# Performance work log

Measured on AMD Instinct MI355X. Metric: run time of the kernel, lower is better.

The kernel has to match this reference:

```python
import jax, jax.numpy as jnp
import numpy as np

B, T, C, H = 2, 2048, 1024, 16
HD = C // H
MAX_WAVELENGTH = 10000.0


def apply_rope(x, positions):
    # x: [B, H, T, HD], positions: [T]
    fraction = 2.0 * jnp.arange(HD // 2, dtype=jnp.float32) / HD
    timescale = MAX_WAVELENGTH ** fraction  # [HD//2]
    sinusoid = positions[:, None] / timescale[None, :]  # [T, HD//2]
    sin = jnp.sin(sinusoid)
    cos = jnp.cos(sinusoid)
    first, second = jnp.split(x, 2, axis=-1)
    out = jnp.concatenate(
        [first * cos - second * sin, second * cos + first * sin], axis=-1
    )
    return out.astype(x.dtype)


def setup_inputs() -> dict:
    key = jax.random.key(0)
    k1, k2, k3 = jax.random.split(key, 3)
    x = jax.random.normal(k1, (B, T, C), dtype=jnp.float32)
    w_attn = jax.random.normal(k2, (C, 3 * C), dtype=jnp.float32) * 0.02
    b_attn = jnp.zeros((3 * C,), dtype=jnp.float32)
    w_proj = jax.random.normal(k3, (C, C), dtype=jnp.float32) * 0.02
    b_proj = jnp.zeros((C,), dtype=jnp.float32)
    return {"x": x, "w_attn": w_attn, "b_attn": b_attn,
            "w_proj": w_proj, "b_proj": b_proj}


def reference(x, w_attn, b_attn, w_proj, b_proj):
    b, t, c = x.shape
    qkv = x @ w_attn + b_attn  # [B, T, 3C]
    q, k, v = jnp.split(qkv, 3, axis=-1)
    q = q.reshape(b, t, H, HD).transpose(0, 2, 1, 3)  # [B, H, T, HD]
    k = k.reshape(b, t, H, HD).transpose(0, 2, 1, 3)
    v = v.reshape(b, t, H, HD).transpose(0, 2, 1, 3)
    positions = jnp.arange(t, dtype=x.dtype)
    q = apply_rope(q, positions)
    k = apply_rope(k, positions)
    att = jnp.einsum('bhqd,bhkd->bhqk', q, k) * (1.0 / jnp.sqrt(HD))
    causal = jnp.tril(jnp.ones((t, t), dtype=bool))
    att = jnp.where(causal, att, jnp.finfo(att.dtype).min)
    att = jax.nn.softmax(att, axis=-1)
    y = jnp.einsum('bhqk,bhkd->bhqd', att, v)
    y = y.transpose(0, 2, 1, 3).reshape(b, t, c)
    return y @ w_proj + b_proj
```

## Files before the change

kernel.cpp:

```cpp
#include <hip/hip_runtime.h>
#include <hip/hip_bf16.h>


typedef __attribute__((ext_vector_type(8))) short short8;
typedef __attribute__((ext_vector_type(4))) float floatx4;

__device__ __forceinline__ unsigned short f2bf(float f) {
    union { float f; unsigned int u; } v; v.f = f;
    unsigned int r = v.u + 0x7FFFu + ((v.u >> 16) & 1u);
    return (unsigned short)(r >> 16);
}

__device__ __forceinline__ float bf2f(unsigned short u) {
    union { unsigned int u; float f; } v; v.u = ((unsigned int)u) << 16;
    return v.f;
}

__device__ __forceinline__ unsigned int pk2bf(float a, float b) {
    union { float f; unsigned int u; } ua, ub;
    ua.f = a; ub.f = b;
    return __builtin_amdgcn_perm(ub.u + 0x8000u, ua.u + 0x8000u, 0x07060302u);
}

__device__ __forceinline__ void gld16(const void* g, void* l) {
    __builtin_amdgcn_global_load_lds(
        (const __attribute__((address_space(1))) unsigned int*)g,
        (__attribute__((address_space(3))) unsigned int*)l, 16, 0, 0);
}

__global__ void cast_f32_bf16(const float* __restrict__ in,
                              unsigned short* __restrict__ out, int n4) {
    int i = blockIdx.x * blockDim.x + threadIdx.x;
    if (i < n4) {
        float4 v = ((const float4*)in)[i];
        ushort4 o;
        o.x = f2bf(v.x); o.y = f2bf(v.y); o.z = f2bf(v.z); o.w = f2bf(v.w);
        ((ushort4*)out)[i] = o;
    }
}

__global__ void transpose_cast(const float* __restrict__ in,
                               unsigned short* __restrict__ out,
                               int R, int NC) {
    __shared__ unsigned short tile[64][65];
    int r0 = blockIdx.y * 64;
    int c0 = blockIdx.x * 64;
    int t = threadIdx.x;
    int col = t & 63;
    int rr = t >> 6;
#pragma unroll
    for (int i = 0; i < 16; i++) {
        int row = rr + i * 4;
        tile[row][col] = f2bf(in[(size_t)(r0 + row) * NC + c0 + col]);
    }
    __syncthreads();
#pragma unroll
    for (int i = 0; i < 16; i++) {
        int orow = rr + i * 4;
        out[(size_t)(c0 + orow) * R + r0 + col] = tile[col][orow];
    }
}

template <int OUT_BF16>
__global__ __launch_bounds__(256) void gemm_lds(
    const unsigned short* __restrict__ A,
    const unsigned short* __restrict__ BT,
    const float* __restrict__ bias,
    void* __restrict__ out,
    int M, int N, int K) {
    __shared__ __align__(16) unsigned short as[128 * 64];
    __shared__ __align__(16) unsigned short bs[128 * 64];
    int lane = threadIdx.x & 63;
    int w = threadIdx.x >> 6;
    int wx = w & 1, wy = w >> 1;
    int l16 = lane & 15, quad = lane >> 4;
    int m0 = blockIdx.y * 128;
    int n0 = blockIdx.x * 128;
    int x = l16 & 7;
    int lr = lane >> 3;
    int gc = (lane & 7) ^ lr;

    floatx4 acc[4][4];
#pragma unroll
    for (int mi = 0; mi < 4; mi++)
#pragma unroll
        for (int ni = 0; ni < 4; ni++)
            acc[mi][ni] = (floatx4){0.f, 0.f, 0.f, 0.f};

    for (int k0 = 0; k0 < K; k0 += 64) {
        __syncthreads();
#pragma unroll
        for (int i = 0; i < 4; i++) {
            int seg = w * 4 + i;
            int row = seg * 8 + lr;
            gld16(A + (size_t)(m0 + row) * K + k0 + gc * 8, &as[seg * 512]);
            gld16(BT + (size_t)(n0 + row) * K + k0 + gc * 8, &bs[seg * 512]);
        }
        __syncthreads();
#pragma unroll
        for (int kk = 0; kk < 2; kk++) {
            short8 af[4], bf[4];
#pragma unroll
            for (int mi = 0; mi < 4; mi++) {
                int r = wy * 64 + mi * 16 + l16;
                af[mi] = *(const short8*)&as[r * 64 + (((kk << 2) | quad) ^ x) * 8];
            }
#pragma unroll
            for (int ni = 0; ni < 4; ni++) {
                int r = wx * 64 + ni * 16 + l16;
                bf[ni] = *(const short8*)&bs[r * 64 + (((kk << 2) | quad) ^ x) * 8];
            }
#pragma unroll
            for (int mi = 0; mi < 4; mi++)
#pragma unroll
                for (int ni = 0; ni < 4; ni++)
                    acc[mi][ni] = __builtin_amdgcn_mfma_f32_16x16x32_bf16(
                        af[mi], bf[ni], acc[mi][ni], 0, 0, 0);
        }
    }

#pragma unroll
    for (int mi = 0; mi < 4; mi++)
#pragma unroll
        for (int ni = 0; ni < 4; ni++) {
            int row = m0 + wy * 64 + mi * 16 + quad * 4;
            int col = n0 + wx * 64 + ni * 16 + l16;
            float bv = bias[col];
#pragma unroll
            for (int r = 0; r < 4; r++) {
                float v = acc[mi][ni][r] + bv;
                if (OUT_BF16)
                    ((unsigned short*)out)[(size_t)(row + r) * N + col] = f2bf(v);
                else
                    ((float*)out)[(size_t)(row + r) * N + col] = v;
            }
        }
}

__global__ void rope_reorg(const unsigned short* __restrict__ qkv,
                           unsigned short* __restrict__ qT,
                           unsigned short* __restrict__ kT) {
    int idx = blockIdx.x * 256 + threadIdx.x;
    int d = idx & 31;
    int h = (idx >> 5) & 15;
    int bt = idx >> 9;
    int t = bt & 2047;
    int b = bt >> 11;
    const unsigned short* row = qkv + (size_t)bt * 3072;
    float q1 = bf2f(row[h * 64 + d]);
    float q2 = bf2f(row[h * 64 + d + 32]);
    float k1 = bf2f(row[1024 + h * 64 + d]);
    float k2 = bf2f(row[1024 + h * 64 + d + 32]);
    float inv_ts = exp2f(-0.41524101186092036f * (float)d);
    float ang = (float)t * inv_ts;
    float s = sinf(ang), c = cosf(ang);
    size_t obase = ((size_t)(b * 16 + h) * 2048 + t) * 64 + d;
    qT[obase]      = f2bf((q1 * c - q2 * s) * 0.125f);
    qT[obase + 32] = f2bf((q2 * c + q1 * s) * 0.125f);
    kT[obase]      = f2bf(k1 * c - k2 * s);
    kT[obase + 32] = f2bf(k2 * c + k1 * s);
}

__global__ void v_transpose(const unsigned short* __restrict__ qkv,
                            unsigned short* __restrict__ vT) {
    __shared__ unsigned short tile[64][65];
    int bh = blockIdx.y;
    int b = bh >> 4, h = bh & 15;
    int t0 = blockIdx.x * 64;
    int tid = threadIdx.x;
    int col = tid & 63;
    int rr = tid >> 6;
#pragma unroll
    for (int i = 0; i < 16; i++) {
        int trow = rr + i * 4;
        tile[trow][col] =
            qkv[(size_t)(b * 2048 + t0 + trow) * 3072 + 2048 + h * 64 + col];
    }
    __syncthreads();
#pragma unroll
    for (int i = 0; i < 16; i++) {
        int drow = rr + i * 4;
        vT[((size_t)bh * 64 + drow) * 2048 + t0 + col] = tile[col][drow];
    }
}

__global__ __launch_bounds__(512) void attn4(
    const unsigned short* __restrict__ qT,
    const unsigned short* __restrict__ kT,
    const unsigned short* __restrict__ vT,
    unsigned short* __restrict__ y) {
    __shared__ __align__(16) unsigned short kbuf[2][64 * 64];
    __shared__ __align__(16) unsigned short vbuf[2][64 * 64];
    __shared__ __align__(16) unsigned short pl[8][16 * 88];
    int lane = threadIdx.x & 63;
    int w = threadIdx.x >> 6;
    int l16 = lane & 15, quad = lane >> 4;
    int blk = blockIdx.x;
    int idx = blk >> 5;
    int qb = (idx < 8) ? (15 - idx * 2) : ((idx - 8) * 2);
    int bh = blk & 31;
    int b = bh >> 4, h = bh & 15;
    int q0 = qb * 128 + w * 16;
    int dt = 2 * qb + (w >> 2);
    const unsigned short* qp = qT + (size_t)bh * 2048 * 64;
    const unsigned short* kp = kT + (size_t)bh * 2048 * 64;
    const unsigned short* vp = vT + (size_t)bh * 64 * 2048;
    unsigned short* plw = pl[w];
    int x = l16 & 7;

    short8 qf0 = *(const short8*)(qp + (size_t)(q0 + l16) * 64 + quad * 8);
    short8 qf1 = *(const short8*)(qp + (size_t)(q0 + l16) * 64 + 32 + quad * 8);

    floatx4 acc[4];
#pragma unroll
    for (int ni = 0; ni < 4; ni++) acc[ni] = (floatx4){0.f, 0.f, 0.f, 0.f};
    float l_part = 0.f;

    auto stage = [&](int bi, int j0) {
#pragma unroll
        for (int i = 0; i < 2; i++) {
            int t = w * 2 + i;
            if (t < 8) {
                int r = t * 8 + (lane >> 3);
                int c = (lane & 7) ^ (r & 7);
                gld16(kp + (size_t)(j0 + r) * 64 + c * 8, &kbuf[bi][t * 512]);
            } else {
                int s = t - 8;
                int d = s * 8 + (lane >> 3);
                int c = (lane & 7) ^ (d & 7);
                gld16(vp + (size_t)d * 2048 + j0 + c * 8, &vbuf[bi][s * 512]);
            }
        }
    };

    int L = 2 * qb + 2;
    stage(0, 0);
    for (int it = 0; it < L; it++) {
        int j0 = it * 64;
        int bi = it & 1;
        __syncthreads();
        if (it + 1 < L) stage(bi ^ 1, j0 + 64);
        if (it > dt) continue;
        const unsigned short* kb = kbuf[bi];
        const unsigned short* vb = vbuf[bi];
        bool diag = (it == dt);
        floatx4 s[4];
#pragma unroll
        for (int c = 0; c < 4; c++) {
            int r = c * 16 + l16;
            short8 kf0 = *(const short8*)&kb[r * 64 + ((quad) ^ x) * 8];
            short8 kf1 = *(const short8*)&kb[r * 64 + ((quad | 4) ^ x) * 8];
            floatx4 z = (floatx4){0.f, 0.f, 0.f, 0.f};
            z = __builtin_amdgcn_mfma_f32_16x16x32_bf16(kf0, qf0, z, 0, 0, 0);
            z = __builtin_amdgcn_mfma_f32_16x16x32_bf16(kf1, qf1, z, 0, 0, 0);
            s[c] = z;
        }
        int query = q0 + l16;
#pragma unroll
        for (int c = 0; c < 4; c++) {
            float p[4];
#pragma unroll
            for (int r = 0; r < 4; r++) {
                float e = __expf(s[c][r]);
                if (diag) {
                    int key = j0 + c * 16 + quad * 4 + r;
                    e = (key <= query) ? e : 0.f;
                }
                p[r] = e;
            }
            l_part += (p[0] + p[1]) + (p[2] + p[3]);
            uint2 pk = {pk2bf(p[0], p[1]), pk2bf(p[2], p[3])};
            *(uint2*)&plw[l16 * 88 + c * 16 + quad * 4] = pk;
        }
        short8 pa0 = *(const short8*)&plw[l16 * 88 + quad * 8];
        short8 pa1 = *(const short8*)&plw[l16 * 88 + 32 + quad * 8];
#pragma unroll
        for (int ni = 0; ni < 4; ni++) {
            int d = ni * 16 + l16;
            short8 vf0 = *(const short8*)&vb[d * 64 + ((quad) ^ x) * 8];
            short8 vf1 = *(const short8*)&vb[d * 64 + ((quad | 4) ^ x) * 8];
            acc[ni] = __builtin_amdgcn_mfma_f32_16x16x32_bf16(pa0, vf0, acc[ni], 0, 0, 0);
            acc[ni] = __builtin_amdgcn_mfma_f32_16x16x32_bf16(pa1, vf1, acc[ni], 0, 0, 0);
        }
    }

    float tot = l_part;
    tot += __shfl_xor(tot, 16, 64);
    tot += __shfl_xor(tot, 32, 64);
    float inv[4];
#pragma unroll
    for (int r = 0; r < 4; r++)
        inv[r] = 1.f / __shfl(tot, quad * 4 + r, 16);
#pragma unroll
    for (int ni = 0; ni < 4; ni++)
#pragma unroll
        for (int r = 0; r < 4; r++) {
            int t = q0 + quad * 4 + r;
            y[((size_t)(b * 2048 + t)) * 1024 + h * 64 + ni * 16 + l16] =
                f2bf(acc[ni][r] * inv[r]);
        }
}

extern "C" void kernel_launch(void* const* d_in, const int* in_sizes, int n_in,
                              void* d_out, int out_size, void* d_ws, size_t ws_size,
                              hipStream_t stream) {
    const float* x      = (const float*)d_in[0];
    const float* w_attn = (const float*)d_in[1];
    const float* b_attn = (const float*)d_in[2];
    const float* w_proj = (const float*)d_in[3];
    const float* b_proj = (const float*)d_in[4];
    float* out = (float*)d_out;

    char* ws = (char*)d_ws;
    unsigned short* x_bf = (unsigned short*)ws;
    unsigned short* wTa  = (unsigned short*)(ws + (8ull << 20));
    unsigned short* wTp  = (unsigned short*)(ws + (14ull << 20));
    unsigned short* qkv  = (unsigned short*)(ws + (16ull << 20));
    unsigned short* qTb  = (unsigned short*)(ws + (40ull << 20));
    unsigned short* kTb  = (unsigned short*)(ws + (48ull << 20));
    unsigned short* vTb  = (unsigned short*)(ws + (56ull << 20));
    unsigned short* y_bf = x_bf;

    cast_f32_bf16<<<4096, 256, 0, stream>>>(x, x_bf, 1048576);
    transpose_cast<<<dim3(48, 16), 256, 0, stream>>>(w_attn, wTa, 1024, 3072);
    transpose_cast<<<dim3(16, 16), 256, 0, stream>>>(w_proj, wTp, 1024, 1024);
    gemm_lds<1><<<dim3(24, 32), 256, 0, stream>>>(x_bf, wTa, b_attn, qkv,
                                                  4096, 3072, 1024);
    rope_reorg<<<8192, 256, 0, stream>>>(qkv, qTb, kTb);
    v_transpose<<<dim3(32, 32), 256, 0, stream>>>(qkv, vTb);
    attn4<<<512, 512, 0, stream>>>(qTb, kTb, vTb, y_bf);
    gemm_lds<0><<<dim3(8, 32), 256, 0, stream>>>(y_bf, wTp, b_proj, out,
                                                 4096, 1024, 1024);
}
```

Measured before the change: 201.0 us.

## Fuse RoPE and V transpose into QKV GEMM epilogue; narrow proj tiles

The QKV GEMM epilogue now applies the bias, RoPE (using a precomputed sin/cos table) and the q scaling, and writes Q and K straight into per-head layout. V is transposed through LDS and written as vT. This removes the intermediate qkv buffer and the separate rope_reorg and v_transpose kernels. The output projection GEMM switches to 128x64 tiles so that 512 blocks launch instead of 256, which improves CU occupancy. A small rope_tab kernel is added, and the fused epilogue uses scattered 2-byte stores for Q and K.

Measured after the change: 190.1 us. 1.06x faster.

```diff
diff --git a/kernel.cpp b/kernel.cpp
--- a/kernel.cpp
+++ b/kernel.cpp
@@ -11,11 +11,6 @@
     return (unsigned short)(r >> 16);
 }
 
-__device__ __forceinline__ float bf2f(unsigned short u) {
-    union { unsigned int u; float f; } v; v.u = ((unsigned int)u) << 16;
-    return v.f;
-}
-
 __device__ __forceinline__ unsigned int pk2bf(float a, float b) {
     union { float f; unsigned int u; } ua, ub;
     ua.f = a; ub.f = b;
@@ -26,6 +21,14 @@
     __builtin_amdgcn_global_load_lds(
         (const __attribute__((address_space(1))) unsigned int*)g,
         (__attribute__((address_space(3))) unsigned int*)l, 16, 0, 0);
+}
+
+__global__ void rope_tab(float2* __restrict__ tab) {
+    int i = blockIdx.x * 256 + threadIdx.x;
+    int t = i >> 5, d = i & 31;
+    float inv_ts = exp2f(-0.41524101186092036f * (float)d);
+    float ang = (float)t * inv_ts;
+    tab[i] = make_float2(sinf(ang), cosf(ang));
 }
 
 __global__ void cast_f32_bf16(const float* __restrict__ in,
@@ -61,17 +64,20 @@
     }
 }
 
-template <int OUT_BF16>
-__global__ __launch_bounds__(256) void gemm_lds(
+__global__ __launch_bounds__(256) void gemm_qkv(
     const unsigned short* __restrict__ A,
     const unsigned short* __restrict__ BT,
     const float* __restrict__ bias,
-    void* __restrict__ out,
-    int M, int N, int K) {
-    __shared__ __align__(16) unsigned short as[128 * 64];
-    __shared__ __align__(16) unsigned short bs[128 * 64];
-    int lane = threadIdx.x & 63;
-    int w = threadIdx.x >> 6;
+    const float2* __restrict__ tab,
+    unsigned short* __restrict__ qT,
+    unsigned short* __restrict__ kT,
+    unsigned short* __restrict__ vT) {
+    __shared__ __align__(16) unsigned short smem[16384];
+    unsigned short* as = smem;
+    unsigned short* bs = smem + 8192;
+    int tid = threadIdx.x;
+    int lane = tid & 63;
+    int w = tid >> 6;
     int wx = w & 1, wy = w >> 1;
     int l16 = lane & 15, quad = lane >> 4;
     int m0 = blockIdx.y * 128;
@@ -87,14 +93,14 @@
         for (int ni = 0; ni < 4; ni++)
             acc[mi][ni] = (floatx4){0.f, 0.f, 0.f, 0.f};
 
-    for (int k0 = 0; k0 < K; k0 += 64) {
+    for (int k0 = 0; k0 < 1024; k0 += 64) {
         __syncthreads();
 #pragma unroll
         for (int i = 0; i < 4; i++) {
             int seg = w * 4 + i;
             int row = seg * 8 + lr;
-            gld16(A + (size_t)(m0 + row) * K + k0 + gc * 8, &as[seg * 512]);
-            gld16(BT + (size_t)(n0 + row) * K + k0 + gc * 8, &bs[seg * 512]);
+            gld16(A + (size_t)(m0 + row) * 1024 + k0 + gc * 8, &as[seg * 512]);
+            gld16(BT + (size_t)(n0 + row) * 1024 + k0 + gc * 8, &bs[seg * 512]);
         }
         __syncthreads();
 #pragma unroll
@@ -119,69 +125,135 @@
         }
     }
 
+    int region = n0 >> 10;
+    int b = m0 >> 11;
+    float b0 = bias[n0 + wx * 64 + l16];
+    float b1 = bias[n0 + wx * 64 + 16 + l16];
+    float b2 = bias[n0 + wx * 64 + 32 + l16];
+    float b3 = bias[n0 + wx * 64 + 48 + l16];
+
+    if (region < 2) {
+        unsigned short* qk = region ? kT : qT;
+        float scale = region ? 1.0f : 0.125f;
+        int h = ((n0 & 1023) + wx * 64) >> 6;
+        unsigned short* obase = qk + (size_t)(b * 16 + h) * 2048 * 64;
+#pragma unroll
+        for (int mi = 0; mi < 4; mi++)
+#pragma unroll
+            for (int r = 0; r < 4; r++) {
+                int t = (m0 & 2047) + wy * 64 + mi * 16 + quad * 4 + r;
+                float2 sc0 = tab[t * 32 + l16];
+                float2 sc1 = tab[t * 32 + 16 + l16];
+                float v1 = acc[mi][0][r] + b0, v2 = acc[mi][2][r] + b2;
+                float w1 = acc[mi][1][r] + b1, w2 = acc[mi][3][r] + b3;
+                unsigned short* orow = obase + (size_t)t * 64;
+                orow[l16]      = f2bf((v1 * sc0.y - v2 * sc0.x) * scale);
+                orow[l16 + 32] = f2bf((v2 * sc0.y + v1 * sc0.x) * scale);
+                orow[l16 + 16] = f2bf((w1 * sc1.y - w2 * sc1.x) * scale);
+                orow[l16 + 48] = f2bf((w2 * sc1.y + w1 * sc1.x) * scale);
+            }
+    } else {
+        __syncthreads();
+#pragma unroll
+        for (int mi = 0; mi < 4; mi++)
+#pragma unroll
+            for (int ni = 0; ni < 4; ni++) {
+                int d_loc = wx * 64 + ni * 16 + l16;
+                int t_base = wy * 64 + mi * 16 + quad * 4;
+                float bv = (ni == 0) ? b0 : (ni == 1) ? b1 : (ni == 2) ? b2 : b3;
+                uint2 pk;
+                pk.x = pk2bf(acc[mi][ni][0] + bv, acc[mi][ni][1] + bv);
+                pk.y = pk2bf(acc[mi][ni][2] + bv, acc[mi][ni][3] + bv);
+                int e = d_loc * 128 + (t_base ^ ((d_loc & 15) << 3));
+                *(uint2*)&smem[e] = pk;
+            }
+        __syncthreads();
+        int d_r = tid >> 1, half = tid & 1;
+        int cv = (n0 - 2048) + d_r;
+        int hh = cv >> 6, dd = cv & 63;
+        int fofs = (d_r & 15) << 3;
+        size_t vbase = ((size_t)(b * 16 + hh) * 64 + dd) * 2048 + (m0 & 2047);
+#pragma unroll
+        for (int c = 0; c < 8; c++) {
+            int tc = half * 64 + c * 8;
+            short8 val = *(const short8*)&smem[d_r * 128 + (tc ^ fofs)];
+            *(short8*)&vT[vbase + tc] = val;
+        }
+    }
+}
+
+__global__ __launch_bounds__(256) void gemm_proj(
+    const unsigned short* __restrict__ A,
+    const unsigned short* __restrict__ BT,
+    const float* __restrict__ bias,
+    float* __restrict__ out) {
+    __shared__ __align__(16) unsigned short as[128 * 64];
+    __shared__ __align__(16) unsigned short bs[64 * 64];
+    int lane = threadIdx.x & 63;
+    int w = threadIdx.x >> 6;
+    int wx = w & 1, wy = w >> 1;
+    int l16 = lane & 15, quad = lane >> 4;
+    int m0 = blockIdx.y * 128;
+    int n0 = blockIdx.x * 64;
+    int x = l16 & 7;
+    int lr = lane >> 3;
+    int gc = (lane & 7) ^ lr;
+
+    floatx4 acc[4][2];
 #pragma unroll
     for (int mi = 0; mi < 4; mi++)
 #pragma unroll
-        for (int ni = 0; ni < 4; ni++) {
+        for (int ni = 0; ni < 2; ni++)
+            acc[mi][ni] = (floatx4){0.f, 0.f, 0.f, 0.f};
+
+    for (int k0 = 0; k0 < 1024; k0 += 64) {
+        __syncthreads();
+#pragma unroll
+        for (int i = 0; i < 6; i++) {
+            int seg = w * 6 + i;
+            if (seg < 16) {
+                int row = seg * 8 + lr;
+                gld16(A + (size_t)(m0 + row) * 1024 + k0 + gc * 8, &as[seg * 512]);
+            } else {
+                int s2 = seg - 16;
+                int row = s2 * 8 + lr;
+                gld16(BT + (size_t)(n0 + row) * 1024 + k0 + gc * 8, &bs[s2 * 512]);
+            }
+        }
+        __syncthreads();
+#pragma unroll
+        for (int kk = 0; kk < 2; kk++) {
+            short8 af[4], bf[2];
+#pragma unroll
+            for (int mi = 0; mi < 4; mi++) {
+                int r = wy * 64 + mi * 16 + l16;
+                af[mi] = *(const short8*)&as[r * 64 + (((kk << 2) | quad) ^ x) * 8];
+            }
+#pragma unroll
+            for (int ni = 0; ni < 2; ni++) {
+                int r = wx * 32 + ni * 16 + l16;
+                bf[ni] = *(const short8*)&bs[r * 64 + (((kk << 2) | quad) ^ x) * 8];
+            }
+#pragma unroll
+            for (int mi = 0; mi < 4; mi++)
+#pragma unroll
+                for (int ni = 0; ni < 2; ni++)
+                    acc[mi][ni] = __builtin_amdgcn_mfma_f32_16x16x32_bf16(
+                        af[mi], bf[ni], acc[mi][ni], 0, 0, 0);
+        }
+    }
+
+#pragma unroll
+    for (int mi = 0; mi < 4; mi++)
+#pragma unroll
+        for (int ni = 0; ni < 2; ni++) {
             int row = m0 + wy * 64 + mi * 16 + quad * 4;
-            int col = n0 + wx * 64 + ni * 16 + l16;
+            int col = n0 + wx * 32 + ni * 16 + l16;
             float bv = bias[col];
 #pragma unroll
-            for (int r = 0; r < 4; r++) {
-                float v = acc[mi][ni][r] + bv;
-                if (OUT_BF16)
-                    ((unsigned short*)out)[(size_t)(row + r) * N + col] = f2bf(v);
-                else
-                    ((float*)out)[(size_t)(row + r) * N + col] = v;
-            }
-        }
-}
-
-__global__ void rope_reorg(const unsigned short* __restrict__ qkv,
-                           unsigned short* __restrict__ qT,
-                           unsigned short* __restrict__ kT) {
-    int idx = blockIdx.x * 256 + threadIdx.x;
-    int d = idx & 31;
-    int h = (idx >> 5) & 15;
-    int bt = idx >> 9;
-    int t = bt & 2047;
-    int b = bt >> 11;
-    const unsigned short* row = qkv + (size_t)bt * 3072;
-    float q1 = bf2f(row[h * 64 + d]);
-    float q2 = bf2f(row[h * 64 + d + 32]);
-    float k1 = bf2f(row[1024 + h * 64 + d]);
-    float k2 = bf2f(row[1024 + h * 64 + d + 32]);
-    float inv_ts = exp2f(-0.41524101186092036f * (float)d);
-    float ang = (float)t * inv_ts;
-    float s = sinf(ang), c = cosf(ang);
-    size_t obase = ((size_t)(b * 16 + h) * 2048 + t) * 64 + d;
-    qT[obase]      = f2bf((q1 * c - q2 * s) * 0.125f);
-    qT[obase + 32] = f2bf((q2 * c + q1 * s) * 0.125f);
-    kT[obase]      = f2bf(k1 * c - k2 * s);
-    kT[obase + 32] = f2bf(k2 * c + k1 * s);
-}
-
-__global__ void v_transpose(const unsigned short* __restrict__ qkv,
-                            unsigned short* __restrict__ vT) {
-    __shared__ unsigned short tile[64][65];
-    int bh = blockIdx.y;
-    int b = bh >> 4, h = bh & 15;
-    int t0 = blockIdx.x * 64;
-    int tid = threadIdx.x;
-    int col = tid & 63;
-    int rr = tid >> 6;
-#pragma unroll
-    for (int i = 0; i < 16; i++) {
-        int trow = rr + i * 4;
-        tile[trow][col] =
-            qkv[(size_t)(b * 2048 + t0 + trow) * 3072 + 2048 + h * 64 + col];
-    }
-    __syncthreads();
-#pragma unroll
-    for (int i = 0; i < 16; i++) {
-        int drow = rr + i * 4;
-        vT[((size_t)bh * 64 + drow) * 2048 + t0 + col] = tile[col][drow];
-    }
+            for (int r = 0; r < 4; r++)
+                out[(size_t)(row + r) * 1024 + col] = acc[mi][ni][r] + bv;
+        }
 }
 
 __global__ __launch_bounds__(512) void attn4(
@@ -315,20 +387,18 @@
     unsigned short* x_bf = (unsigned short*)ws;
     unsigned short* wTa  = (unsigned short*)(ws + (8ull << 20));
     unsigned short* wTp  = (unsigned short*)(ws + (14ull << 20));
-    unsigned short* qkv  = (unsigned short*)(ws + (16ull << 20));
-    unsigned short* qTb  = (unsigned short*)(ws + (40ull << 20));
-    unsigned short* kTb  = (unsigned short*)(ws + (48ull << 20));
-    unsigned short* vTb  = (unsigned short*)(ws + (56ull << 20));
+    unsigned short* qTb  = (unsigned short*)(ws + (16ull << 20));
+    unsigned short* kTb  = (unsigned short*)(ws + (24ull << 20));
+    unsigned short* vTb  = (unsigned short*)(ws + (32ull << 20));
+    float2*         tab  = (float2*)(ws + (40ull << 20));
     unsigned short* y_bf = x_bf;
 
+    rope_tab<<<256, 256, 0, stream>>>(tab);
     cast_f32_bf16<<<4096, 256, 0, stream>>>(x, x_bf, 1048576);
     transpose_cast<<<dim3(48, 16), 256, 0, stream>>>(w_attn, wTa, 1024, 3072);
     transpose_cast<<<dim3(16, 16), 256, 0, stream>>>(w_proj, wTp, 1024, 1024);
-    gemm_lds<1><<<dim3(24, 32), 256, 0, stream>>>(x_bf, wTa, b_attn, qkv,
-                                                  4096, 3072, 1024);
-    rope_reorg<<<8192, 256, 0, stream>>>(qkv, qTb, kTb);
-    v_transpose<<<dim3(32, 32), 256, 0, stream>>>(qkv, vTb);
+    gemm_qkv<<<dim3(24, 32), 256, 0, stream>>>(x_bf, wTa, b_attn, tab,
+                                               qTb, kTb, vTb);
     attn4<<<512, 512, 0, stream>>>(qTb, kTb, vTb, y_bf);
-    gemm_lds<0><<<dim3(8, 32), 256, 0, stream>>>(y_bf, wTp, b_proj, out,
-                                                 4096, 1024, 1024);
-}
+    gemm_proj<<<dim3(16, 32), 256, 0, stream>>>(y_bf, wTp, b_proj, out);
+}
```
